# Performance work log

Measured on AMD Instinct MI355X. Metric: run time of the kernel, lower is better.

The kernel has to match this reference:

```python
import jax, jax.numpy as jnp
import numpy as np
from functools import partial

BN_EPS = 1e-5

def conv2d(x, w, pad):
    # x: [N,C,H,W], w: [O,I,kh,kw]
    return jax.lax.conv_general_dilated(
        x, w, window_strides=(1, 1), padding=((pad, pad), (pad, pad)),
        dimension_numbers=("NCHW", "OIHW", "NCHW"))

def bn_prelu(x, gamma, beta, mean, var, alpha):
    # eval-mode BatchNorm2d followed by single-parameter PReLU
    scale = gamma * jax.lax.rsqrt(var + BN_EPS)
    h = x * scale[None, :, None, None] + (beta - mean * scale)[None, :, None, None]
    return jnp.where(h >= 0, h, alpha * h)

def unfold3x3(x):
    # torch nn.Unfold(3, padding=1): output layout [N, C*9, H*W]
    N, C, H, W = x.shape
    xp = jnp.pad(x, ((0, 0), (0, 0), (1, 1), (1, 1)))
    patches = jnp.stack(
        [xp[:, :, i:i + H, j:j + W] for i in range(3) for j in range(3)],
        axis=2)  # [N, C, 9, H, W] -- row-major identical to [N, C*9, H*W]
    return patches

def setup_inputs() -> dict:
    key = jax.random.key(0)
    ks = jax.random.split(key, 16)
    N, C, H, W = 16, 256, 64, 64
    K2 = 9
    inp = {
        "x": jax.random.normal(ks[0], (N, C, H, W), jnp.float32),
        "y": jax.random.normal(ks[1], (N, C, H, W), jnp.float32),
        # gernerate_kernel_spatial[0]: Conv3x3 C->C + BN + PReLU
        "W1": jax.random.normal(ks[2], (C, C, 3, 3), jnp.float32) * 0.05,
        "g1": jax.random.normal(ks[3], (C,), jnp.float32) * 0.1 + 1.0,
        "b1": jax.random.normal(ks[4], (C,), jnp.float32) * 0.1,
        "m1": jax.random.normal(ks[5], (C,), jnp.float32) * 0.1,
        "v1": jax.random.uniform(ks[6], (C,), jnp.float32, 0.5, 1.5),
        "a1": jnp.float32(0.25),
        # gernerate_kernel_spatial[1]: Conv1x1 C->9 + BN + PReLU
        "W2": jax.random.normal(ks[7], (K2, C, 1, 1), jnp.float32) * 0.05,
        "g2": jax.random.normal(ks[8], (K2,), jnp.float32) * 0.1 + 1.0,
        "b2": jax.random.normal(ks[9], (K2,), jnp.float32) * 0.1,
        "m2": jax.random.normal(ks[10], (K2,), jnp.float32) * 0.1,
        "v2": jax.random.uniform(ks[11], (K2,), jnp.float32, 0.5, 1.5),
        "a2": jnp.float32(0.25),
    }
    return inp

def reference(x, y, W1, g1, b1, m1, v1, a1, W2, g2, b2, m2, v2, a2):
    N, C, H, W = x.shape
    # dynamic per-pixel 3x3 kernel from y: [N, 9, H, W]
    h = bn_prelu(conv2d(y, W1, pad=1), g1, b1, m1, v1, a1)
    kernel = bn_prelu(conv2d(h, W2, pad=0), g2, b2, m2, v2, a2)
    # kernel.reshape(N,9,H,W,1).permute(0,2,3,1,4) -> [N,H,W,9]
    kern = jnp.transpose(kernel, (0, 2, 3, 1))
    # unfold(x) is [N, C*9, H*W]; torch reshapes it ROW-MAJOR to [N,H,W,C,9]
    ux = unfold3x3(x).reshape(N, H, W, C, 9)
    # matmul [N,H,W,C,9] @ [N,H,W,9,1] -> squeeze -> permute to NCHW
    out = jnp.einsum("nhwck,nhwk->nchw", ux, kern)
    return out
```

## Files before the change

kernel.cpp:

```cpp
#include <hip/hip_runtime.h>
#include <hip/hip_bf16.h>

typedef __attribute__((ext_vector_type(8))) short bf16x8;
typedef __attribute__((ext_vector_type(4))) float f32x4;
typedef __attribute__((ext_vector_type(8))) unsigned short u16x8;
typedef __attribute__((ext_vector_type(4))) unsigned short u16x4;

#define BN_EPS 1e-5f

__device__ __forceinline__ unsigned short f2bf(float f) {
  unsigned int u = __float_as_uint(f);
  unsigned int r = u + 0x7FFFu + ((u >> 16) & 1u);
  return (unsigned short)(r >> 16);
}
__device__ __forceinline__ float bf2f(unsigned short u) {
  union { float f; unsigned int i; } v; v.i = ((unsigned int)u) << 16; return v.f;
}

__device__ __forceinline__ void async_ld16(const unsigned short* g, unsigned short* l) {
  __builtin_amdgcn_global_load_lds(
      (const __attribute__((address_space(1))) void*)g,
      (__attribute__((address_space(3))) void*)l, 16, 0, 0);
}

__global__ __launch_bounds__(256) void params_kernel(
    const float* __restrict__ g1, const float* __restrict__ b1,
    const float* __restrict__ m1, const float* __restrict__ v1,
    const float* __restrict__ W2, const float* __restrict__ g2,
    const float* __restrict__ b2, const float* __restrict__ m2,
    const float* __restrict__ v2,
    float* __restrict__ bias1, float* __restrict__ W2f, float* __restrict__ bias2)
{
  int t = threadIdx.x;
  {
    float s = g1[t] * rsqrtf(v1[t] + BN_EPS);
    bias1[t] = b1[t] - m1[t] * s;
  }
  for (int i = t; i < 2304; i += 256) {
    int j = i >> 8;
    float s2 = g2[j] * rsqrtf(v2[j] + BN_EPS);
    W2f[i] = W2[i] * s2;
  }
  if (t < 9) {
    float s2 = g2[t] * rsqrtf(v2[t] + BN_EPS);
    bias2[t] = b2[t] - m2[t] * s2;
  }
}

__global__ __launch_bounds__(256) void fold_w1_kernel(
    const float* __restrict__ W1, const float* __restrict__ g1,
    const float* __restrict__ v1, unsigned short* __restrict__ Bt)
{
  int o = blockIdx.x;
  int t = threadIdx.x;
  float s = g1[o] * rsqrtf(v1[o] + BN_EPS);
  const float* src = W1 + (size_t)o * 2304 + (size_t)t * 9;
  float wv[9];
  #pragma unroll
  for (int tap = 0; tap < 9; ++tap) wv[tap] = src[tap] * s;
  unsigned short* dst = Bt + (size_t)o * 2304 + t;
  #pragma unroll
  for (int tap = 0; tap < 9; ++tap) dst[tap * 256] = f2bf(wv[tap]);
}

__global__ __launch_bounds__(256) void border_zero_kernel(unsigned short* __restrict__ yTp)
{
  int n = blockIdx.x, t = threadIdx.x;
  size_t base = (size_t)n * 66 * 66 * 256;
  u16x8 z = (u16x8){0, 0, 0, 0, 0, 0, 0, 0};
  for (int i = t; i < 2112; i += 256) {
    *(u16x8*)(yTp + base + (size_t)i * 8) = z;
    *(u16x8*)(yTp + base + (size_t)65 * 66 * 256 + (size_t)i * 8) = z;
  }
  for (int i = t; i < 2048; i += 256) {
    int hh = 1 + (i >> 5);
    int off = (i & 31) * 8;
    *(u16x8*)(yTp + base + ((size_t)hh * 66 + 0) * 256 + off) = z;
    *(u16x8*)(yTp + base + ((size_t)hh * 66 + 65) * 256 + off) = z;
  }
}

__global__ __launch_bounds__(256) void transpose_pad_kernel(
    const float* __restrict__ y, unsigned short* __restrict__ yTp)
{
  __shared__ unsigned short T[64][68];
  int t = threadIdx.x;
  int nb = blockIdx.x; int n = nb >> 6, h = nb & 63;
  int w4 = (t & 15) * 4;
  int cl = t >> 4;
  for (int cb = 0; cb < 4; ++cb) {
    __syncthreads();
    #pragma unroll
    for (int r = 0; r < 4; ++r) {
      int c = cb * 64 + cl + r * 16;
      float4 v = *(const float4*)(y + ((((size_t)n * 256 + c) * 64 + h) << 6) + w4);
      u16x4 pv = { f2bf(v.x), f2bf(v.y), f2bf(v.z), f2bf(v.w) };
      *(u16x4*)&T[cl + r * 16][w4] = pv;
    }
    __syncthreads();
    size_t base = (((size_t)n * 66 + (h + 1)) * 66 + 1) * 256 + cb * 64;
    #pragma unroll
    for (int pass = 0; pass < 2; ++pass) {
      int w = pass * 32 + (t >> 3);
      int c8 = (t & 7) * 8;
      u16x8 o;
      #pragma unroll
      for (int i = 0; i < 8; ++i) o[i] = T[c8 + i][w];
      *(u16x8*)(yTp + base + (size_t)w * 256 + c8) = o;
    }
  }
}

__global__ __launch_bounds__(256, 2) void conv3x3_mfma_kernel(
    const unsigned short* __restrict__ yTp, const unsigned short* __restrict__ Bt,
    const float* __restrict__ bias1, const float* __restrict__ a1p,
    unsigned short* __restrict__ hT)
{
  __shared__ unsigned short Als[4][4][66][8];
  __shared__ unsigned short Bls[4][256][8];
  int tid = threadIdx.x;
  int w = tid >> 6, l = tid & 63;
  int lr = l & 15, quad = l >> 4;
  int wm = w >> 1, wn = w & 1;
  int bm = blockIdx.x;
  int n = bm >> 5, hb = (bm & 31) * 2;

  f32x4 acc[4][8];
  #pragma unroll
  for (int im = 0; im < 4; ++im)
    #pragma unroll
    for (int in_ = 0; in_ < 8; ++in_)
      acc[im][in_] = (f32x4){0.f, 0.f, 0.f, 0.f};

  const size_t nb66 = (size_t)n * 66;

  for (int chunk = 0; chunk < 8; ++chunk) {
    int ci0 = chunk * 32;
    #pragma unroll 1
    for (int tap = 0; tap < 9; ++tap) {
      int ti = tap / 3;
      int tj = tap - 3 * ti;
      __syncthreads();
      if (tap == 0) {
        const unsigned short* ga =
            yTp + (((nb66 + hb + w) * 66 + l) << 8) + ci0;
        #pragma unroll
        for (int q = 0; q < 4; ++q)
          async_ld16(ga + q * 8, &Als[q][w][0][0]);
        if (tid < 32) {
          int q = tid >> 3, rr = (tid >> 1) & 3, pxl = 64 + (tid & 1);
          u16x8 v = *(const u16x8*)(
              yTp + (((nb66 + hb + rr) * 66 + pxl) << 8) + ci0 + q * 8);
          *(u16x8*)&Als[q][rr][pxl][0] = v;
        }
      }
      const unsigned short* gb =
          Bt + (size_t)(w * 64 + l) * 2304 + tap * 256 + ci0;
      #pragma unroll
      for (int q = 0; q < 4; ++q)
        async_ld16(gb + q * 8, &Bls[q][w * 64][0]);
      __syncthreads();
      bf16x8 af[4], bfr[8];
      #pragma unroll
      for (int im = 0; im < 4; ++im)
        af[im] = *(const bf16x8*)&Als[quad][wm + ti][im * 16 + lr + tj][0];
      #pragma unroll
      for (int in_ = 0; in_ < 8; ++in_)
        bfr[in_] = *(const bf16x8*)&Bls[quad][wn * 128 + in_ * 16 + lr][0];
      #pragma unroll
      for (int im = 0; im < 4; ++im)
        #pragma unroll
        for (int in_ = 0; in_ < 8; ++in_)
          acc[im][in_] = __builtin_amdgcn_mfma_f32_16x16x32_bf16(
              af[im], bfr[in_], acc[im][in_], 0, 0, 0);
    }
  }

  float a1 = a1p[0];
  size_t pix0 = (size_t)bm * 128 + wm * 64;
  #pragma unroll
  for (int in_ = 0; in_ < 8; ++in_) {
    int c = wn * 128 + in_ * 16 + lr;
    float bs = bias1[c];
    #pragma unroll
    for (int im = 0; im < 4; ++im) {
      size_t m0 = pix0 + im * 16 + quad * 4;
      #pragma unroll
      for (int r = 0; r < 4; ++r) {
        float v = acc[im][in_][r] + bs;
        v = (v >= 0.f) ? v : a1 * v;
        hT[(m0 + r) * 256 + c] = f2bf(v);
      }
    }
  }
}

__global__ __launch_bounds__(256) void conv1x1_kernel(
    const unsigned short* __restrict__ hT, const float* __restrict__ W2f,
    const float* __restrict__ bias2, const float* __restrict__ a2p,
    float* __restrict__ kernP)
{
  __shared__ float w2s[2304];
  int t = threadIdx.x;
  for (int i = t; i < 2304; i += 256) w2s[i] = W2f[i];
  __syncthreads();
  int seg = t & 3;
  int pr = t >> 2;
  int p = blockIdx.x * 64 + pr;
  const unsigned short* hp = hT + (size_t)p * 256;
  float acc[9];
  #pragma unroll
  for (int j = 0; j < 9; ++j) acc[j] = 0.f;
  for (int c0 = seg * 8; c0 < 256; c0 += 32) {
    u16x8 hv = *(const u16x8*)(hp + c0);
    float hf[8];
    #pragma unroll
    for (int i = 0; i < 8; ++i) hf[i] = bf2f(hv[i]);
    #pragma unroll
    for (int j = 0; j < 9; ++j)
      #pragma unroll
      for (int i = 0; i < 8; ++i)
        acc[j] = fmaf(hf[i], w2s[j * 256 + c0 + i], acc[j]);
  }
  #pragma unroll
  for (int j = 0; j < 9; ++j) {
    acc[j] += __shfl_xor(acc[j], 1);
    acc[j] += __shfl_xor(acc[j], 2);
  }
  if (seg == 0) {
    float a2 = a2p[0];
    #pragma unroll
    for (int j = 0; j < 9; ++j) {
      float v = acc[j] + bias2[j];
      v = (v >= 0.f) ? v : a2 * v;
      kernP[j * 65536 + p] = v;
    }
  }
}

__global__ __launch_bounds__(256) void apply_dyn_kernel(
    const float* __restrict__ x, const float* __restrict__ kernP,
    float* __restrict__ out)
{
  __shared__ float xs[64 * 65];
  __shared__ float ks[9][16];
  int t = threadIdx.x;
  int b = blockIdx.x;
  int g = b & 3;
  int nh = b >> 2;
  int n = nh >> 6, hp = nh & 63;
  int c = 4 * hp + g;

  const float* xplane = x + (((size_t)n * 256 + c) << 12);
  for (int i = t; i < 1024; i += 256) {
    float4 v = *(const float4*)(xplane + i * 4);
    int row = i >> 4;
    int col = (i * 4) & 63;
    float* d = &xs[row * 65 + col];
    d[0] = v.x; d[1] = v.y; d[2] = v.z; d[3] = v.w;
  }
  int pbase = n * 4096 + hp * 64 + g * 16;
  for (int i = t; i < 144; i += 256)
    ks[i / 16][i & 15] = kernP[(i / 16) * 65536 + pbase + (i & 15)];
  __syncthreads();

  int s = t & 15;
  int crow = t >> 4;
  float ksr[9];
  #pragma unroll
  for (int k2 = 0; k2 < 9; ++k2) ksr[k2] = ks[k2][s];

  int r0base = s * 2304 + crow * 9;
  #pragma unroll 4
  for (int jj = 0; jj < 16; ++jj) {
    int cp = crow + 16 * jj;
    int r0 = r0base + 144 * jj;
    float acc = 0.f;
    #pragma unroll
    for (int k2 = 0; k2 < 9; ++k2) {
      int r = r0 + k2;
      int k = r >> 12;
      int rem = r & 4095;
      int h = rem >> 6;
      int w = rem & 63;
      int ti = k / 3;
      int tj = k - 3 * ti;
      int hh = h + ti - 1;
      int ww = w + tj - 1;
      float xv = 0.f;
      if ((unsigned)hh < 64u && (unsigned)ww < 64u) xv = xs[hh * 65 + ww];
      acc = fmaf(xv, ksr[k2], acc);
    }
    out[(((size_t)n * 256 + cp) << 12) + (hp << 6) + g * 16 + s] = acc;
  }
}

extern "C" void kernel_launch(void* const* d_in, const int* in_sizes, int n_in,
                              void* d_out, int out_size, void* d_ws, size_t ws_size,
                              hipStream_t stream) {
  const float* x  = (const float*)d_in[0];
  const float* y  = (const float*)d_in[1];
  const float* W1 = (const float*)d_in[2];
  const float* g1 = (const float*)d_in[3];
  const float* b1 = (const float*)d_in[4];
  const float* m1 = (const float*)d_in[5];
  const float* v1 = (const float*)d_in[6];
  const float* a1 = (const float*)d_in[7];
  const float* W2 = (const float*)d_in[8];
  const float* g2 = (const float*)d_in[9];
  const float* b2 = (const float*)d_in[10];
  const float* m2 = (const float*)d_in[11];
  const float* v2 = (const float*)d_in[12];
  const float* a2 = (const float*)d_in[13];
  float* out = (float*)d_out;

  char* ws = (char*)d_ws;
  size_t off = 0;
  const size_t yTp_bytes = (size_t)16 * 66 * 66 * 256 * 2;
  unsigned short* yTp = (unsigned short*)(ws + off); off += yTp_bytes;
  unsigned short* Bt  = (unsigned short*)(ws + off); off += (size_t)589824 * 2;
  unsigned short* hT  = (unsigned short*)(ws + off); off += (size_t)16777216 * 2;
  float* kernP = (float*)(ws + off); off += (size_t)589824 * 4;
  float* bias1 = (float*)(ws + off); off += 1024;
  float* W2f   = (float*)(ws + off); off += 9216;
  float* bias2 = (float*)(ws + off); off += 64;

  params_kernel<<<1, 256, 0, stream>>>(g1, b1, m1, v1, W2, g2, b2, m2, v2,
                                       bias1, W2f, bias2);
  fold_w1_kernel<<<256, 256, 0, stream>>>(W1, g1, v1, Bt);
  border_zero_kernel<<<16, 256, 0, stream>>>(yTp);
  transpose_pad_kernel<<<1024, 256, 0, stream>>>(y, yTp);
  conv3x3_mfma_kernel<<<512, 256, 0, stream>>>(yTp, Bt, bias1, a1, hT);
  conv1x1_kernel<<<1024, 256, 0, stream>>>(hT, W2f, bias2, a2, kernP);
  apply_dyn_kernel<<<4096, 256, 0, stream>>>(x, kernP, out);
}
```

Measured before the change: 365.9 us.

## Double-buffer conv3x3 LDS staging and simplify dynamic-kernel apply indexing

The conv3x3 MFMA kernel now double-buffers its A and B LDS tiles. The next tap or chunk is prefetched asynchronously while the current one computes, which cuts the loop from two barriers per tap to one. The apply kernel pads its shared x plane with a zero border and walks incremental addresses instead of recomputing div/mod and bounds checks per element. The cost is double the LDS in conv3x3, which may limit occupancy under launch_bounds(256,2), plus more complex address bookkeeping in the apply kernel.

Result: no change. 368.3 us (+0.7%).

```diff
diff --git a/kernel.cpp b/kernel.cpp
--- a/kernel.cpp
+++ b/kernel.cpp
@@ -116,8 +116,8 @@
     const float* __restrict__ bias1, const float* __restrict__ a1p,
     unsigned short* __restrict__ hT)
 {
-  __shared__ unsigned short Als[4][4][66][8];
-  __shared__ unsigned short Bls[4][256][8];
+  __shared__ unsigned short Als[2][4][4][66][8];
+  __shared__ unsigned short Bls[2][4][256][8];
   int tid = threadIdx.x;
   int w = tid >> 6, l = tid & 63;
   int lr = l & 15, quad = l >> 4;
@@ -133,47 +133,60 @@
       acc[im][in_] = (f32x4){0.f, 0.f, 0.f, 0.f};
 
   const size_t nb66 = (size_t)n * 66;
-
-  for (int chunk = 0; chunk < 8; ++chunk) {
-    int ci0 = chunk * 32;
+  const unsigned short* gaRow = yTp + (((nb66 + hb + w) * 66) << 8);
+  const unsigned short* gb0 = Bt + (size_t)(w * 64 + l) * 2304;
+
+  auto stageA = [&](int chunk, int buf) {
+    const unsigned short* ga = gaRow + ((size_t)l << 8) + chunk * 32;
+    #pragma unroll
+    for (int q = 0; q < 4; ++q)
+      async_ld16(ga + q * 8, &Als[buf][q][w][0][0]);
+    if (l < 2) {
+      const unsigned short* ga2 = gaRow + ((size_t)(64 + l) << 8) + chunk * 32;
+      #pragma unroll
+      for (int q = 0; q < 4; ++q)
+        async_ld16(ga2 + q * 8, &Als[buf][q][w][64][0]);
+    }
+  };
+  auto stageB = [&](int tap, int chunk, int buf) {
+    const unsigned short* gb = gb0 + tap * 256 + chunk * 32;
+    #pragma unroll
+    for (int q = 0; q < 4; ++q)
+      async_ld16(gb + q * 8, &Bls[buf][q][w * 64][0]);
+  };
+
+  stageA(0, 0);
+  stageB(0, 0, 0);
+  __syncthreads();
+
+  int ab = 0, bb = 0;
+  #pragma unroll 1
+  for (int c = 0; c < 8; ++c) {
     #pragma unroll 1
-    for (int tap = 0; tap < 9; ++tap) {
-      int ti = tap / 3;
-      int tj = tap - 3 * ti;
-      __syncthreads();
-      if (tap == 0) {
-        const unsigned short* ga =
-            yTp + (((nb66 + hb + w) * 66 + l) << 8) + ci0;
-        #pragma unroll
-        for (int q = 0; q < 4; ++q)
-          async_ld16(ga + q * 8, &Als[q][w][0][0]);
-        if (tid < 32) {
-          int q = tid >> 3, rr = (tid >> 1) & 3, pxl = 64 + (tid & 1);
-          u16x8 v = *(const u16x8*)(
-              yTp + (((nb66 + hb + rr) * 66 + pxl) << 8) + ci0 + q * 8);
-          *(u16x8*)&Als[q][rr][pxl][0] = v;
-        }
-      }
-      const unsigned short* gb =
-          Bt + (size_t)(w * 64 + l) * 2304 + tap * 256 + ci0;
-      #pragma unroll
-      for (int q = 0; q < 4; ++q)
-        async_ld16(gb + q * 8, &Bls[q][w * 64][0]);
-      __syncthreads();
+    for (int t = 0; t < 9; ++t) {
+      if (t == 0 && c < 7) stageA(c + 1, ab ^ 1);
+      if (t < 8) stageB(t + 1, c, bb ^ 1);
+      else if (c < 7) stageB(0, c + 1, bb ^ 1);
+
+      int ti = t / 3, tj = t - 3 * ti;
       bf16x8 af[4], bfr[8];
       #pragma unroll
       for (int im = 0; im < 4; ++im)
-        af[im] = *(const bf16x8*)&Als[quad][wm + ti][im * 16 + lr + tj][0];
+        af[im] = *(const bf16x8*)&Als[ab][quad][wm + ti][im * 16 + lr + tj][0];
       #pragma unroll
       for (int in_ = 0; in_ < 8; ++in_)
-        bfr[in_] = *(const bf16x8*)&Bls[quad][wn * 128 + in_ * 16 + lr][0];
+        bfr[in_] = *(const bf16x8*)&Bls[bb][quad][wn * 128 + in_ * 16 + lr][0];
       #pragma unroll
       for (int im = 0; im < 4; ++im)
         #pragma unroll
         for (int in_ = 0; in_ < 8; ++in_)
           acc[im][in_] = __builtin_amdgcn_mfma_f32_16x16x32_bf16(
               af[im], bfr[in_], acc[im][in_], 0, 0, 0);
-    }
+
+      __syncthreads();
+      bb ^= 1;
+    }
+    ab ^= 1;
   }
 
   float a1 = a1p[0];
@@ -242,7 +255,7 @@
     const float* __restrict__ x, const float* __restrict__ kernP,
     float* __restrict__ out)
 {
-  __shared__ float xs[64 * 65];
+  __shared__ float xs[66 * 67];
   __shared__ float ks[9][16];
   int t = threadIdx.x;
   int b = blockIdx.x;
@@ -255,10 +268,12 @@
   for (int i = t; i < 1024; i += 256) {
     float4 v = *(const float4*)(xplane + i * 4);
     int row = i >> 4;
-    int col = (i * 4) & 63;
-    float* d = &xs[row * 65 + col];
+    int col = (i & 15) * 4;
+    float* d = &xs[(row + 1) * 67 + col + 1];
     d[0] = v.x; d[1] = v.y; d[2] = v.z; d[3] = v.w;
   }
+  if (t < 67) { xs[t] = 0.f; xs[65 * 67 + t] = 0.f; }
+  if (t < 128) { int r = (t >> 1) + 1; int cc = (t & 1) * 65; xs[r * 67 + cc] = 0.f; }
   int pbase = n * 4096 + hp * 64 + g * 16;
   for (int i = t; i < 144; i += 256)
     ks[i / 16][i & 15] = kernP[(i / 16) * 65536 + pbase + (i & 15)];
@@ -270,28 +285,30 @@
   #pragma unroll
   for (int k2 = 0; k2 < 9; ++k2) ksr[k2] = ks[k2][s];
 
-  int r0base = s * 2304 + crow * 9;
+  int r0 = s * 2304 + crow * 144;
+  int k0 = r0 >> 12;
+  int rem0 = r0 & 4095;
+  int wcol = rem0 & 63;
+  int ti0 = (k0 >= 6) ? 2 : ((k0 >= 3) ? 1 : 0);
+  int tj0 = k0 - 3 * ti0;
+  int addr = (rem0 >> 6) * 67 + wcol + ti0 * 67 + tj0;
+  int cnt = 4096 - rem0;
+  int kN = k0 + 1;
+  int tiN = (kN >= 6) ? 2 : ((kN >= 3) ? 1 : 0);
+  int addrAtCross = tiN * 67 + (kN - 3 * tiN);
+
+  size_t outIdx = (((size_t)n * 256 + crow * 16) << 12) + (hp << 6) + g * 16 + s;
   #pragma unroll 4
-  for (int jj = 0; jj < 16; ++jj) {
-    int cp = crow + 16 * jj;
-    int r0 = r0base + 144 * jj;
+  for (int oi = 0; oi < 16; ++oi) {
     float acc = 0.f;
     #pragma unroll
     for (int k2 = 0; k2 < 9; ++k2) {
-      int r = r0 + k2;
-      int k = r >> 12;
-      int rem = r & 4095;
-      int h = rem >> 6;
-      int w = rem & 63;
-      int ti = k / 3;
-      int tj = k - 3 * ti;
-      int hh = h + ti - 1;
-      int ww = w + tj - 1;
-      float xv = 0.f;
-      if ((unsigned)hh < 64u && (unsigned)ww < 64u) xv = xs[hh * 65 + ww];
-      acc = fmaf(xv, ksr[k2], acc);
-    }
-    out[(((size_t)n * 256 + cp) << 12) + (hp << 6) + g * 16 + s] = acc;
+      acc = fmaf(xs[addr], ksr[k2], acc);
+      ++wcol; ++addr;
+      if (wcol == 64) { wcol = 0; addr += 3; }
+      if (--cnt == 0) addr = addrAtCross;
+    }
+    out[outIdx + ((size_t)oi << 12)] = acc;
   }
 }
 
```
